# Optimization experiments

Measured on AMD Instinct MI355X. Metric: run time of the kernel, lower is better.

Reference implementation:

```python
import jax, jax.numpy as jnp
import numpy as np

ZETA = 1.1
GAMMA = -0.1

B, F, D = 1024, 32, 128


def setup_inputs() -> dict:
    key = jax.random.key(0)
    k1, k2 = jax.random.split(key)
    feature = jax.random.normal(k1, (B, F, D), dtype=jnp.float32)
    # nn.Parameter init: normal(mean=0, std=0.001)
    matrix = jax.random.normal(k2, (F, F, D, D), dtype=jnp.float32) * 0.001
    return {"feature": feature, "matrix": matrix}


def reference(feature, matrix):
    # feature: [B, F, D]; matrix (logAlpha of hard-concrete gate): [F, F, D, D]
    nF = matrix.shape[0]
    # strict upper-triangular pair mask over (i, j)
    mask = jnp.triu(jnp.ones((nF, nF), dtype=feature.dtype), k=1)
    # deterministic (eval-mode) hard-concrete gate: stretch + clamp
    s = jax.nn.sigmoid(matrix)
    z = jnp.clip(s * (ZETA - GAMMA) + GAMMA, 0.0, 1.0)
    l0_out = mask[:, :, None, None] * z  # [F, F, D, D]
    # out[b,i,j] = f_i^T Z_ij f_j  == sum_{d,e} f[b,i,d] * Z[i,j,d,e] * f[b,j,e]
    # (faithful to: (f[:, :, None, :, None] @ f[:, None, :, None, :]) * Z, summed over (d, e))
    out = jnp.einsum('bid,ijde,bje->bij', feature, l0_out, feature)
    return out
```

## Files before the change

kernel.cpp:

```cpp
#include <hip/hip_runtime.h>

#define B_SZ 1024
#define F_SZ 32
#define D_SZ 128
#define FD   (F_SZ * D_SZ)
#define LDA  136
#define LDB  136

typedef __bf16 bf16x8 __attribute__((ext_vector_type(8)));
typedef float floatx4 __attribute__((ext_vector_type(4)));

__device__ __forceinline__ unsigned short f2bf(float f) {
  unsigned u = __float_as_uint(f);
  u += 0x7fffu + ((u >> 16) & 1u);
  return (unsigned short)(u >> 16);
}

__device__ __forceinline__ float bf2f(unsigned short h) {
  return __uint_as_float(((unsigned)h) << 16);
}

__global__ __launch_bounds__(256, 2)
void interaction_pair_kernel(const float* __restrict__ feat,
                             const float* __restrict__ mat,
                             float* __restrict__ out) {
  __shared__ unsigned short sA[128 * LDA];
  __shared__ unsigned short sBT[128 * LDB];

  const int t    = threadIdx.x;
  const int w    = t >> 6;
  const int lane = t & 63;
  const int l15  = lane & 15;
  const int quad = lane >> 4;

  int p = blockIdx.x;
  int i = 0;
  while (p >= F_SZ - 1 - i) { p -= F_SZ - 1 - i; ++i; }
  const int j = i + 1 + p;

  {
    const float* zp = mat + (((size_t)i * F_SZ + j) * (size_t)(D_SZ * D_SZ));
    #pragma unroll 8
    for (int it = 0; it < 64; ++it) {
      int idx = it * 256 + t;
      int d = idx >> 7, e = idx & 127;
      float v = zp[idx];
      float s = 1.0f / (1.0f + __expf(-v));
      float z = fminf(1.0f, fmaxf(0.0f, fmaf(s, 1.2f, -0.1f)));
      sBT[e * LDB + d] = f2bf(z);
    }
  }

  for (int bt = 0; bt < 8; ++bt) {
    const int b0 = bt * 128;

    #pragma unroll 4
    for (int it = 0; it < 16; ++it) {
      int idx4 = it * 256 + t;
      int r = idx4 >> 5, c4 = idx4 & 31;
      const float4 v = *(const float4*)(feat + (size_t)(b0 + r) * FD + i * D_SZ + c4 * 4);
      ushort4 h;
      h.x = f2bf(v.x); h.y = f2bf(v.y); h.z = f2bf(v.z); h.w = f2bf(v.w);
      *(ushort4*)(&sA[r * LDA + c4 * 4]) = h;
    }
    __syncthreads();

    floatx4 acc[2][8];
    #pragma unroll
    for (int mf = 0; mf < 2; ++mf)
      #pragma unroll
      for (int nf = 0; nf < 8; ++nf)
        acc[mf][nf] = (floatx4){0.f, 0.f, 0.f, 0.f};

    #pragma unroll
    for (int k0 = 0; k0 < 128; k0 += 32) {
      const int kc = k0 + quad * 8;
      bf16x8 a0 = *(const bf16x8*)&sA[(w * 32 +      l15) * LDA + kc];
      bf16x8 a1 = *(const bf16x8*)&sA[(w * 32 + 16 + l15) * LDA + kc];
      #pragma unroll
      for (int nf = 0; nf < 8; ++nf) {
        bf16x8 bfr = *(const bf16x8*)&sBT[(nf * 16 + l15) * LDB + kc];
        acc[0][nf] = __builtin_amdgcn_mfma_f32_16x16x32_bf16(a0, bfr, acc[0][nf], 0, 0, 0);
        acc[1][nf] = __builtin_amdgcn_mfma_f32_16x16x32_bf16(a1, bfr, acc[1][nf], 0, 0, 0);
      }
    }

    #pragma unroll
    for (int mf = 0; mf < 2; ++mf) {
      float pl[4] = {0.f, 0.f, 0.f, 0.f};
      const int rb = w * 32 + mf * 16 + quad * 4;
      #pragma unroll
      for (int nf = 0; nf < 8; ++nf) {
        const int col = nf * 16 + l15;
        const float* fj = feat + (size_t)(b0 + rb) * FD + j * D_SZ + col;
        floatx4 c = acc[mf][nf];
        pl[0] += c[0] * fj[0];
        pl[1] += c[1] * fj[FD];
        pl[2] += c[2] * fj[2 * FD];
        pl[3] += c[3] * fj[3 * FD];
      }
      #pragma unroll
      for (int off = 1; off < 16; off <<= 1) {
        pl[0] += __shfl_xor(pl[0], off, 64);
        pl[1] += __shfl_xor(pl[1], off, 64);
        pl[2] += __shfl_xor(pl[2], off, 64);
        pl[3] += __shfl_xor(pl[3], off, 64);
      }
      if (l15 == 0) {
        size_t ob = (size_t)(b0 + rb) * (F_SZ * F_SZ) + (size_t)i * F_SZ + j;
        out[ob]                    = pl[0];
        out[ob + 1 * F_SZ * F_SZ]  = pl[1];
        out[ob + 2 * F_SZ * F_SZ]  = pl[2];
        out[ob + 3 * F_SZ * F_SZ]  = pl[3];
      }
    }
    __syncthreads();
  }
}

extern "C" void kernel_launch(void* const* d_in, const int* in_sizes, int n_in,
                              void* d_out, int out_size, void* d_ws, size_t ws_size,
                              hipStream_t stream) {
  const float* feat = (const float*)d_in[0];
  const float* mat  = (const float*)d_in[1];
  float* out = (float*)d_out;

  hipMemsetAsync(out, 0, (size_t)out_size * sizeof(float), stream);

  const int n_pairs = F_SZ * (F_SZ - 1) / 2;
  interaction_pair_kernel<<<dim3(n_pairs), dim3(256), 0, stream>>>(feat, mat, out);
}
```

Measured before the change: 145.2 us.

## Precompute bf16 gate and feature buffers, then split batch across 4x more blocks

Splits the work into three kernels. Two prep kernels write the transposed bf16 gate matrix and a bf16 copy of the features to workspace. A pair GEMM kernel then loads its gate fragments straight into registers, reads bf16 A tiles directly from global memory without LDS staging, and spreads the batch over a second grid dimension (496x4 blocks). The aim is to stop the feature tile being converted once per pair and to raise parallelism above 496 blocks, at the cost of extra kernel launches and workspace traffic. The old single kernel is kept as a fallback when the workspace is too small.

```diff
diff --git a/kernel.cpp b/kernel.cpp
--- a/kernel.cpp
+++ b/kernel.cpp
@@ -1,11 +1,9 @@
 #include <hip/hip_runtime.h>
 
-#define B_SZ 1024
 #define F_SZ 32
 #define D_SZ 128
-#define FD   (F_SZ * D_SZ)
-#define LDA  136
-#define LDB  136
+#define FD   4096
+#define NPAIR 496
 
 typedef __bf16 bf16x8 __attribute__((ext_vector_type(8)));
 typedef float floatx4 __attribute__((ext_vector_type(4)));
@@ -16,6 +14,146 @@
   return (unsigned short)(u >> 16);
 }
 
+__device__ __forceinline__ void decode_pair(int p, int& io, int& jo) {
+  int i = 0;
+  while (p >= F_SZ - 1 - i) { p -= F_SZ - 1 - i; ++i; }
+  io = i; jo = i + 1 + p;
+}
+
+__global__ __launch_bounds__(256)
+void prep_z(const float* __restrict__ mat, unsigned short* __restrict__ Zt) {
+  __shared__ unsigned short tile[128 * 136];
+  int i, j; decode_pair(blockIdx.x, i, j);
+  const float* zp = mat + (((size_t)i * F_SZ + j) << 14);
+  const int t = threadIdx.x;
+  #pragma unroll 8
+  for (int it = 0; it < 64; ++it) {
+    int idx = it * 256 + t;
+    int d = idx >> 7, e = idx & 127;
+    float v = zp[idx];
+    float s = 1.0f / (1.0f + __expf(-v));
+    float z = fminf(1.0f, fmaxf(0.0f, fmaf(s, 1.2f, -0.1f)));
+    tile[e * 136 + d] = f2bf(z);
+  }
+  __syncthreads();
+  unsigned short* op = Zt + ((size_t)blockIdx.x << 14);
+  #pragma unroll 4
+  for (int it = 0; it < 16; ++it) {
+    int idx4 = it * 256 + t;
+    int e = idx4 >> 5, d4 = idx4 & 31;
+    ushort4 v = *(const ushort4*)&tile[e * 136 + d4 * 4];
+    *(ushort4*)&op[idx4 * 4] = v;
+  }
+}
+
+__global__ __launch_bounds__(256)
+void prep_f(const float* __restrict__ feat, unsigned short* __restrict__ fb) {
+  int gid = blockIdx.x * 256 + threadIdx.x;
+  #pragma unroll
+  for (int k = 0; k < 4; ++k) {
+    size_t idx = (size_t)k * 262144 + gid;
+    float4 v = *(const float4*)(feat + idx * 4);
+    ushort4 h;
+    h.x = f2bf(v.x); h.y = f2bf(v.y); h.z = f2bf(v.z); h.w = f2bf(v.w);
+    *(ushort4*)(fb + idx * 4) = h;
+  }
+}
+
+__global__ __launch_bounds__(256, 2)
+void pair_gemm(const unsigned short* __restrict__ Zt,
+               const unsigned short* __restrict__ fb,
+               const float* __restrict__ feat,
+               float* __restrict__ out) {
+  __shared__ float sRed[128];
+  int i, j; decode_pair(blockIdx.x, i, j);
+  const int t = threadIdx.x;
+  const int lane = t & 63, l15 = lane & 15, quad = lane >> 4;
+  const int wq = t >> 6, we = wq & 1, wb = wq >> 1;
+
+  bf16x8 Bfrag[4][4];
+  {
+    const unsigned short* zp = Zt + ((size_t)blockIdx.x << 14);
+    #pragma unroll
+    for (int nf = 0; nf < 4; ++nf) {
+      const int col = we * 64 + nf * 16 + l15;
+      #pragma unroll
+      for (int ks = 0; ks < 4; ++ks)
+        Bfrag[nf][ks] = *(const bf16x8*)(zp + col * 128 + ks * 32 + quad * 8);
+    }
+  }
+
+  const int bbase = blockIdx.y * 256;
+  for (int it = 0; it < 2; ++it) {
+    const int b0 = bbase + it * 128;
+    const int rowbase = b0 + wb * 64;
+
+    floatx4 acc[4][4];
+    #pragma unroll
+    for (int mf = 0; mf < 4; ++mf)
+      #pragma unroll
+      for (int nf = 0; nf < 4; ++nf)
+        acc[mf][nf] = (floatx4){0.f, 0.f, 0.f, 0.f};
+
+    #pragma unroll
+    for (int ks = 0; ks < 4; ++ks) {
+      #pragma unroll
+      for (int mf = 0; mf < 4; ++mf) {
+        const unsigned short* ap = fb + (size_t)(rowbase + mf * 16 + l15) * FD
+                                      + i * D_SZ + ks * 32 + quad * 8;
+        bf16x8 A = *(const bf16x8*)ap;
+        #pragma unroll
+        for (int nf = 0; nf < 4; ++nf)
+          acc[mf][nf] = __builtin_amdgcn_mfma_f32_16x16x32_bf16(A, Bfrag[nf][ks], acc[mf][nf], 0, 0, 0);
+      }
+    }
+
+    float pl[4][4];
+    #pragma unroll
+    for (int mf = 0; mf < 4; ++mf) {
+      #pragma unroll
+      for (int r = 0; r < 4; ++r) pl[mf][r] = 0.f;
+      #pragma unroll
+      for (int nf = 0; nf < 4; ++nf) {
+        const int col = we * 64 + nf * 16 + l15;
+        const float* fj = feat + (size_t)(rowbase + mf * 16 + quad * 4) * FD + j * D_SZ + col;
+        floatx4 c = acc[mf][nf];
+        pl[mf][0] += c[0] * fj[0];
+        pl[mf][1] += c[1] * fj[FD];
+        pl[mf][2] += c[2] * fj[2 * FD];
+        pl[mf][3] += c[3] * fj[3 * FD];
+      }
+    }
+    #pragma unroll
+    for (int mf = 0; mf < 4; ++mf)
+      #pragma unroll
+      for (int r = 0; r < 4; ++r)
+        #pragma unroll
+        for (int off = 1; off < 16; off <<= 1)
+          pl[mf][r] += __shfl_xor(pl[mf][r], off, 64);
+
+    if (we == 0 && l15 == 0) {
+      #pragma unroll
+      for (int mf = 0; mf < 4; ++mf)
+        #pragma unroll
+        for (int r = 0; r < 4; ++r)
+          sRed[wb * 64 + mf * 16 + quad * 4 + r] = pl[mf][r];
+    }
+    __syncthreads();
+    if (we == 1 && l15 == 0) {
+      #pragma unroll
+      for (int mf = 0; mf < 4; ++mf)
+        #pragma unroll
+        for (int r = 0; r < 4; ++r) {
+          const int lr = wb * 64 + mf * 16 + quad * 4 + r;
+          out[(size_t)(b0 + lr) * (F_SZ * F_SZ) + i * F_SZ + j] = pl[mf][r] + sRed[lr];
+        }
+    }
+    __syncthreads();
+  }
+}
+
+#define LDA  136
+#define LDB  136
 __device__ __forceinline__ float bf2f(unsigned short h) {
   return __uint_as_float(((unsigned)h) << 16);
 }
@@ -26,20 +164,11 @@
                              float* __restrict__ out) {
   __shared__ unsigned short sA[128 * LDA];
   __shared__ unsigned short sBT[128 * LDB];
-
-  const int t    = threadIdx.x;
-  const int w    = t >> 6;
-  const int lane = t & 63;
-  const int l15  = lane & 15;
-  const int quad = lane >> 4;
-
-  int p = blockIdx.x;
-  int i = 0;
-  while (p >= F_SZ - 1 - i) { p -= F_SZ - 1 - i; ++i; }
-  const int j = i + 1 + p;
-
+  const int t = threadIdx.x;
+  const int w = t >> 6, lane = t & 63, l15 = lane & 15, quad = lane >> 4;
+  int i, j; decode_pair(blockIdx.x, i, j);
   {
-    const float* zp = mat + (((size_t)i * F_SZ + j) * (size_t)(D_SZ * D_SZ));
+    const float* zp = mat + (((size_t)i * F_SZ + j) << 14);
     #pragma unroll 8
     for (int it = 0; it < 64; ++it) {
       int idx = it * 256 + t;
@@ -50,10 +179,8 @@
       sBT[e * LDB + d] = f2bf(z);
     }
   }
-
   for (int bt = 0; bt < 8; ++bt) {
     const int b0 = bt * 128;
-
     #pragma unroll 4
     for (int it = 0; it < 16; ++it) {
       int idx4 = it * 256 + t;
@@ -64,14 +191,12 @@
       *(ushort4*)(&sA[r * LDA + c4 * 4]) = h;
     }
     __syncthreads();
-
     floatx4 acc[2][8];
     #pragma unroll
     for (int mf = 0; mf < 2; ++mf)
       #pragma unroll
       for (int nf = 0; nf < 8; ++nf)
         acc[mf][nf] = (floatx4){0.f, 0.f, 0.f, 0.f};
-
     #pragma unroll
     for (int k0 = 0; k0 < 128; k0 += 32) {
       const int kc = k0 + quad * 8;
@@ -84,7 +209,6 @@
         acc[1][nf] = __builtin_amdgcn_mfma_f32_16x16x32_bf16(a1, bfr, acc[1][nf], 0, 0, 0);
       }
     }
-
     #pragma unroll
     for (int mf = 0; mf < 2; ++mf) {
       float pl[4] = {0.f, 0.f, 0.f, 0.f};
@@ -108,10 +232,10 @@
       }
       if (l15 == 0) {
         size_t ob = (size_t)(b0 + rb) * (F_SZ * F_SZ) + (size_t)i * F_SZ + j;
-        out[ob]                    = pl[0];
-        out[ob + 1 * F_SZ * F_SZ]  = pl[1];
-        out[ob + 2 * F_SZ * F_SZ]  = pl[2];
-        out[ob + 3 * F_SZ * F_SZ]  = pl[3];
+        out[ob]                   = pl[0];
+        out[ob + 1 * F_SZ * F_SZ] = pl[1];
+        out[ob + 2 * F_SZ * F_SZ] = pl[2];
+        out[ob + 3 * F_SZ * F_SZ] = pl[3];
       }
     }
     __syncthreads();
@@ -127,6 +251,16 @@
 
   hipMemsetAsync(out, 0, (size_t)out_size * sizeof(float), stream);
 
-  const int n_pairs = F_SZ * (F_SZ - 1) / 2;
-  interaction_pair_kernel<<<dim3(n_pairs), dim3(256), 0, stream>>>(feat, mat, out);
-}
+  const size_t zt_bytes = (size_t)NPAIR * D_SZ * D_SZ * sizeof(unsigned short);
+  const size_t fb_bytes = (size_t)1024 * FD * sizeof(unsigned short);
+
+  if (ws_size >= zt_bytes + fb_bytes) {
+    unsigned short* Zt = (unsigned short*)d_ws;
+    unsigned short* fbuf = Zt + (size_t)NPAIR * D_SZ * D_SZ;
+    prep_z<<<dim3(NPAIR), dim3(256), 0, stream>>>(mat, Zt);
+    prep_f<<<dim3(1024), dim3(256), 0, stream>>>(feat, fbuf);
+    pair_gemm<<<dim3(NPAIR, 4), dim3(256), 0, stream>>>(Zt, fbuf, feat, out);
+  } else {
+    interaction_pair_kernel<<<dim3(NPAIR), dim3(256), 0, stream>>>(feat, mat, out);
+  }
+}
```

Measured after the change: 171.7 us. +18.3%, slower.
